# Kernel optimization log

Measured on AMD Instinct MI355X. Metric: run time of the kernel, lower is better.

Reference implementation:

```python
import jax, jax.numpy as jnp
import numpy as np

T, B, M = 2048, 256, 32


def setup_inputs() -> dict:
    key = jax.random.key(0)
    k1, k2, k3, k4 = jax.random.split(key, 4)
    emissions = jax.random.normal(k1, (T, B, M), jnp.float32)
    tags = jax.random.randint(k2, (T, B), 0, M)
    # weight divides transition scores -> keep strictly positive
    weight = jax.random.uniform(k3, (T, B), jnp.float32, 0.5, 1.5)
    mask = jnp.ones((T, B), jnp.int32)  # first timestep must be all-on
    transitions = jax.random.normal(k4, (M, M), jnp.float32) * 0.1
    start_transitions = jnp.zeros((M,), jnp.float32)
    end_transitions = jnp.zeros((M,), jnp.float32)
    return {
        "emissions": emissions,
        "tags": tags,
        "weight": weight,
        "mask": mask,
        "transitions": transitions,
        "start_transitions": start_transitions,
        "end_transitions": end_transitions,
    }


def reference(emissions, tags, weight, mask, transitions, start_transitions, end_transitions):
    # emissions: [T,B,M]; tags/weight/mask: [T,B]; reduction='sum' (torch default)
    Tn, Bn, Mn = emissions.shape
    maskb = mask.astype(bool)
    tags = jnp.where(maskb, tags, 1)
    maskf = mask.astype(emissions.dtype)

    # ---- gold-path score (_compute_score) ----
    score = start_transitions[tags[0]]
    score = score + (transitions[tags[:-1], tags[1:]] * maskf[1:] / weight[:-1]).sum(0)
    em_sc = jnp.take_along_axis(emissions, tags[:, :, None], axis=-1)[..., 0] * maskf
    score = score + em_sc.sum(0)
    seq_ends = mask.astype(jnp.int32).sum(0) - 1  # [B]
    last_tags = tags[seq_ends, jnp.arange(Bn)]
    score = score + end_transitions[last_tags]

    # ---- log-partition (_compute_normalizer) via logsumexp-semiring scan ----
    neg_inf = jnp.asarray(-jnp.inf, emissions.dtype)
    log_eye = jnp.where(jnp.eye(Mn, dtype=bool), jnp.zeros((), emissions.dtype), neg_inf)

    alpha0 = start_transitions + emissions[0]  # [B,M]

    def step(alpha, xs):
        em_t, w_t, m_t = xs  # [B,M], [B], [B]
        sc = transitions[None, :, :] / w_t[:, None, None] + em_t[:, None, :]  # [B,M,M]
        sc = jnp.where(m_t[:, None, None], sc, log_eye)  # masked step = identity in log-semiring
        alpha = jax.nn.logsumexp(alpha[:, :, None] + sc, axis=1)
        return alpha, None

    alpha, _ = jax.lax.scan(step, alpha0, (emissions[1:], weight[:-1], maskb[1:]))
    log_Z = jax.nn.logsumexp(alpha + end_transitions, axis=1)  # [B]

    nllh = log_Z - score
    return nllh.sum()
```

## Files before the change

kernel.cpp:

```cpp
#include <hip/hip_runtime.h>
#include <hip/hip_bf16.h>
#include <stdint.h>


#define T_DIM 2048
#define B_DIM 256
#define M_DIM 32
#define CHUNKS 32
#define CLEN 64
#define KSC 184.6649652337873f
#define SBIAS2 12599160.66f

typedef __attribute__((ext_vector_type(8))) short short8;
typedef __attribute__((ext_vector_type(16))) float f32x16;

__device__ __forceinline__ int pack_bf16(float lo, float hi) {
  union { float f; uint32_t u; } a, b;
  a.f = lo; b.f = hi;
  return (int)__builtin_amdgcn_perm(b.u, a.u, 0x07060302u);
}

__device__ __forceinline__ int pack_lo16(int lo, int hi) {
  return (int)__builtin_amdgcn_perm((uint32_t)hi, (uint32_t)lo, 0x05040100u);
}

__device__ __forceinline__ float bcast_lane(float v, int idx) {
  return __int_as_float(__builtin_amdgcn_readlane(__float_as_int(v), idx));
}

__global__ __launch_bounds__(256, 2) void chunk_kernel(
    const float* __restrict__ em, const int* __restrict__ tags,
    const float* __restrict__ wt, const int* __restrict__ mask,
    const float* __restrict__ trans, const float* __restrict__ endt,
    uint32_t* __restrict__ mats, float* __restrict__ offs,
    float* __restrict__ out)
{
  int tid = threadIdx.x;
  int lane = tid & 63;
  int h = lane >> 5;
  int r = lane & 31;
  int wid = blockIdx.x * 4 + (tid >> 6);
  int u0 = 4 * wid;
  int bb = u0 & (B_DIM - 1);
  int c = u0 >> 8;
  int t0 = 1 + c * CLEN;
  int t1 = t0 + CLEN; if (t1 > T_DIM) t1 = T_DIM;

  float tpre[16];
#pragma unroll
  for (int j = 0; j < 8; ++j) {
    int row = ((j < 4) ? j : j + 4) + 4 * h;
    tpre[j]     = trans[row * 32 + r] * KSC;
    tpre[8 + j] = trans[(row + 16) * 32 + r] * KSC;
  }

  int tw = t0 - 1 + lane; if (tw > T_DIM - 1) tw = T_DIM - 1;
  int tmk = t0 + lane; if (tmk > T_DIM - 1) tmk = T_DIM - 1;
  float rwv[4];
  uint64_t mk[4];
  uint64_t valid = (t1 - t0 >= 64) ? ~0ull : ((1ull << (t1 - t0)) - 1ull);
#pragma unroll
  for (int ch = 0; ch < 4; ++ch) {
    rwv[ch] = __builtin_amdgcn_rcpf(wt[tw * B_DIM + bb + ch]);
    mk[ch] = __ballot(mask[tmk * B_DIM + bb + ch] != 0) & valid;
  }

  f32x16 X[4];
#pragma unroll
  for (int p = 0; p < 16; ++p) {
    float v = (((p & 3) + 8 * (p >> 2) + 4 * h) == r) ? 1.f : 0.f;
    X[0][p] = v; X[1][p] = v; X[2][p] = v; X[3][p] = v;
  }
  f32x16 z;
#pragma unroll
  for (int u = 0; u < 16; ++u) z[u] = 0.f;

  float off2[4] = {0.f, 0.f, 0.f, 0.f};

  auto step4 = [&](const float* e4, int s) {
    float rw0 = bcast_lane(rwv[0], s), rw1 = bcast_lane(rwv[1], s);
    float rw2 = bcast_lane(rwv[2], s), rw3 = bcast_lane(rwv[3], s);
    float rw[4] = {rw0, rw1, rw2, rw3};
    union { int i[4]; short8 s8; } af1[4], af2[4], b1[4], b2[4];
#pragma unroll
    for (int ch = 0; ch < 4; ++ch) {
      float e = fmaf(e4[ch], KSC, SBIAS2);
      float qf[16];
#pragma unroll
      for (int j = 0; j < 16; ++j)
        qf[j] = fmaf(tpre[j], rw[ch], e);
#pragma unroll
      for (int u = 0; u < 4; ++u) {
        af1[ch].i[u] = pack_lo16(__float_as_int(qf[2 * u]),     __float_as_int(qf[2 * u + 1]));
        af2[ch].i[u] = pack_lo16(__float_as_int(qf[8 + 2 * u]), __float_as_int(qf[8 + 2 * u + 1]));
      }
    }
#pragma unroll
    for (int ch = 0; ch < 4; ++ch)
#pragma unroll
      for (int u = 0; u < 4; ++u) {
        b1[ch].i[u] = pack_bf16(X[ch][2 * u],     X[ch][2 * u + 1]);
        b2[ch].i[u] = pack_bf16(X[ch][8 + 2 * u], X[ch][8 + 2 * u + 1]);
      }
    f32x16 d[4];
#pragma unroll
    for (int ch = 0; ch < 4; ++ch)
      d[ch] = __builtin_amdgcn_mfma_f32_32x32x16_bf16(af1[ch].s8, b1[ch].s8, z, 0, 0, 0);
#pragma unroll
    for (int ch = 0; ch < 4; ++ch)
      X[ch] = __builtin_amdgcn_mfma_f32_32x32x16_bf16(af2[ch].s8, b2[ch].s8, d[ch], 0, 0, 0);
  };

  auto stepOne = [&](f32x16& Xc, float e_em, float rw) {
    float e = fmaf(e_em, KSC, SBIAS2);
    float qf[16];
#pragma unroll
    for (int j = 0; j < 16; ++j)
      qf[j] = fmaf(tpre[j], rw, e);
    union { int i[4]; short8 s8; } af1, af2, b1_, b2_;
#pragma unroll
    for (int u = 0; u < 4; ++u) {
      af1.i[u] = pack_lo16(__float_as_int(qf[2 * u]),     __float_as_int(qf[2 * u + 1]));
      af2.i[u] = pack_lo16(__float_as_int(qf[8 + 2 * u]), __float_as_int(qf[8 + 2 * u + 1]));
      b1_.i[u] = pack_bf16(Xc[2 * u],     Xc[2 * u + 1]);
      b2_.i[u] = pack_bf16(Xc[8 + 2 * u], Xc[8 + 2 * u + 1]);
    }
    f32x16 d = __builtin_amdgcn_mfma_f32_32x32x16_bf16(af1.s8, b1_.s8, z, 0, 0, 0);
    Xc = __builtin_amdgcn_mfma_f32_32x32x16_bf16(af2.s8, b2_.s8, d, 0, 0, 0);
  };

  auto rescale = [&](f32x16& Xc, float& o2) {
    float mx = Xc[0];
#pragma unroll
    for (int u = 1; u < 16; ++u) mx = fmaxf(mx, Xc[u]);
#pragma unroll
    for (int off = 1; off < 64; off <<= 1) mx = fmaxf(mx, __shfl_xor(mx, off));
    float sc = __builtin_amdgcn_rcpf(mx);
    o2 += __builtin_amdgcn_logf(mx);
#pragma unroll
    for (int u = 0; u < 16; ++u) Xc[u] *= sc;
  };

  bool fast = (t1 - t0 == 64) && (mk[0] == ~0ull) && (mk[1] == ~0ull)
            && (mk[2] == ~0ull) && (mk[3] == ~0ull);

  if (fast) {
    float e[4][4], n[4][4];
#pragma unroll
    for (int ch = 0; ch < 4; ++ch)
#pragma unroll
      for (int u = 0; u < 4; ++u)
        e[ch][u] = em[((size_t)((t0 + 2 * u + h) * B_DIM + bb + ch)) * 32 + r];
    for (int g = 0; g < 8; ++g) {
      int tg = t0 + 8 * (g + 1);
#pragma unroll
      for (int ch = 0; ch < 4; ++ch)
#pragma unroll
        for (int u = 0; u < 4; ++u) {
          int tt = tg + 2 * u + h; if (tt > T_DIM - 1) tt = T_DIM - 1;
          n[ch][u] = em[((size_t)(tt * B_DIM + bb + ch)) * 32 + r];
        }
#pragma unroll
      for (int u = 0; u < 4; ++u) {
        int sA = 8 * g + 2 * u, sB = sA + 1;
        float eA[4], eB[4];
#pragma unroll
        for (int ch = 0; ch < 4; ++ch) {
          float sw = __shfl_xor(e[ch][u], 32);
          eA[ch] = h ? sw : e[ch][u];
          eB[ch] = h ? e[ch][u] : sw;
        }
        step4(eA, sA);
        step4(eB, sB);
      }
#pragma unroll
      for (int ch = 0; ch < 4; ++ch) rescale(X[ch], off2[ch]);
#pragma unroll
      for (int ch = 0; ch < 4; ++ch)
#pragma unroll
        for (int u = 0; u < 4; ++u) e[ch][u] = n[ch][u];
    }
  } else {
    float emv[4], emp[4];
#pragma unroll
    for (int ch = 0; ch < 4; ++ch)
      emv[ch] = em[((size_t)((t0 + h) * B_DIM + bb + ch)) * 32 + r];
    int tpf = t0 + 2 + h; if (tpf > T_DIM - 1) tpf = T_DIM - 1;
#pragma unroll
    for (int ch = 0; ch < 4; ++ch)
      emp[ch] = em[((size_t)(tpf * B_DIM + bb + ch)) * 32 + r];

    for (int it = 0; it < CLEN / 2; ++it) {
      int tn = t0 + 2 * it + 4 + h; if (tn > T_DIM - 1) tn = T_DIM - 1;
      float emn[4];
#pragma unroll
      for (int ch = 0; ch < 4; ++ch)
        emn[ch] = em[((size_t)(tn * B_DIM + bb + ch)) * 32 + r];

      int sA = 2 * it, sB = sA + 1;
#pragma unroll
      for (int ch = 0; ch < 4; ++ch) {
        float sw = __shfl_xor(emv[ch], 32);
        if ((mk[ch] >> sA) & 1)
          stepOne(X[ch], h ? sw : emv[ch], bcast_lane(rwv[ch], sA));
        if ((t0 + sB < t1) && ((mk[ch] >> sB) & 1))
          stepOne(X[ch], h ? emv[ch] : sw, bcast_lane(rwv[ch], sB));
      }

      if ((it & 3) == 3) {
#pragma unroll
        for (int ch = 0; ch < 4; ++ch) rescale(X[ch], off2[ch]);
      }
#pragma unroll
      for (int ch = 0; ch < 4; ++ch) { emv[ch] = emp[ch]; emp[ch] = emn[ch]; }
    }
  }

#pragma unroll
  for (int ch = 0; ch < 4; ++ch) {
    uint32_t* mp = mats + (size_t)(u0 + ch) * 512;
#pragma unroll
    for (int u = 0; u < 8; ++u) {
      int pairIdx = (u & 1) + (u >> 1) * 4 + 2 * h;
      mp[pairIdx * 32 + r] = (uint32_t)pack_bf16(X[ch][2 * u], X[ch][2 * u + 1]);
    }
  }
  if (lane == 0) {
#pragma unroll
    for (int ch = 0; ch < 4; ++ch) offs[u0 + ch] = off2[ch];
  }

  int t = t0 + lane;
  float ssc = 0.f;
  if (t < t1) {
#pragma unroll
    for (int ch = 0; ch < 4; ++ch) {
      int b = bb + ch;
      int mkc  = mask[t * B_DIM + b];
      int mkn  = (t + 1 < T_DIM) ? mask[(t + 1) * B_DIM + b] : 0;
      int tg   = mkc ? tags[t * B_DIM + b] : 1;
      int mkp  = mask[(t - 1) * B_DIM + b];
      int tgp  = mkp ? tags[(t - 1) * B_DIM + b] : 1;
      if (mkc)
        ssc += em[(size_t)(t * B_DIM + b) * 32 + tg]
             + trans[tgp * 32 + tg] * __builtin_amdgcn_rcpf(wt[(t - 1) * B_DIM + b]);
      if (mkc && !mkn) ssc += endt[tg];
    }
  }
#pragma unroll
  for (int off = 32; off; off >>= 1) ssc += __shfl_xor(ssc, off);
  if (lane == 0) atomicAdd(out, -ssc);
}

__global__ __launch_bounds__(64) void combine_kernel(
    const float* __restrict__ em, const int* __restrict__ tags,
    const int* __restrict__ mask, const float* __restrict__ startt,
    const float* __restrict__ endt, const uint32_t* __restrict__ mats,
    const float* __restrict__ offs, float* __restrict__ out)
{
  const float INV_LN2 = 1.44269504088896340736f;
  const float LN2 = 0.69314718055994530942f;
  int lane = threadIdx.x;
  int j = lane & 31;
  int h = lane >> 5;
  int b = blockIdx.x;
  int jp = j >> 1, jh = j & 1;

  float a0 = (startt[j] + em[(size_t)b * 32 + j]) * INV_LN2;
  float c0 = a0;
#pragma unroll
  for (int off = 1; off < 32; off <<= 1) c0 = fmaxf(c0, __shfl_xor(c0, off));
  float av = __builtin_amdgcn_exp2f(a0 - c0);
  float acc = c0;

  const uint4* xr0 = (const uint4*)(mats + (size_t)b * 512 + jp * 32 + 16 * h);
  uint4 nv0 = xr0[0], nv1 = xr0[1];
  float noff = offs[b];

  for (int c = 0; c < CHUNKS; ++c) {
    uint4 v0 = nv0, v1 = nv1;
    float offc = noff;
    int cn = (c + 1 < CHUNKS) ? c + 1 : c;
    const uint4* xrn = (const uint4*)(mats + (size_t)(cn * B_DIM + b) * 512 + jp * 32 + 16 * h);
    nv0 = xrn[0]; nv1 = xrn[1];
    noff = offs[cn * B_DIM + b];

    float x[8];
    uint32_t u0[4] = {v0.x, v0.y, v0.z, v0.w};
    uint32_t u1[4] = {v1.x, v1.y, v1.z, v1.w};
#pragma unroll
    for (int e = 0; e < 4; ++e) {
      uint32_t bits0 = jh ? (u0[e] & 0xFFFF0000u) : (u0[e] << 16);
      uint32_t bits1 = jh ? (u1[e] & 0xFFFF0000u) : (u1[e] << 16);
      union { uint32_t uu; float f; } cv0, cv1;
      cv0.uu = bits0; cv1.uu = bits1;
      x[e] = cv0.f; x[4 + e] = cv1.f;
    }
    float s0 = 0.f, s1 = 0.f;
#pragma unroll
    for (int i = 0; i < 4; ++i) {
      s0 = fmaf(x[i],     __shfl(av, 16 * h + i),     s0);
      s1 = fmaf(x[4 + i], __shfl(av, 16 * h + 4 + i), s1);
    }
    float an = s0 + s1;
    an += __shfl_xor(an, 32);
    float mx = an;
#pragma unroll
    for (int off = 1; off < 32; off <<= 1) mx = fmaxf(mx, __shfl_xor(mx, off));
    av = an * __builtin_amdgcn_rcpf(mx);
    acc += __builtin_amdgcn_logf(mx) + offc;
  }

  float sv = av * __builtin_amdgcn_exp2f(endt[j] * INV_LN2);
#pragma unroll
  for (int off = 1; off < 32; off <<= 1) sv += __shfl_xor(sv, off);
  if (lane == 0) {
    float logZ = (acc + __builtin_amdgcn_logf(sv)) * LN2;
    int mk0 = mask[b];
    int tg0 = mk0 ? tags[b] : 1;
    float s0 = startt[tg0] + (mk0 ? em[(size_t)b * 32 + tg0] : 0.f);
    int mk1 = mask[B_DIM + b];
    if (mk0 && !mk1) s0 += endt[tg0];
    atomicAdd(out, logZ - s0);
  }
}

extern "C" void kernel_launch(void* const* d_in, const int* in_sizes, int n_in,
                              void* d_out, int out_size, void* d_ws, size_t ws_size,
                              hipStream_t stream) {
  const float* em   = (const float*)d_in[0];
  const int*   tags = (const int*)d_in[1];
  const float* wt   = (const float*)d_in[2];
  const int*   mask = (const int*)d_in[3];
  const float* tr   = (const float*)d_in[4];
  const float* stt  = (const float*)d_in[5];
  const float* ent  = (const float*)d_in[6];
  float* out = (float*)d_out;

  float* offs = (float*)d_ws;
  uint32_t* mats = (uint32_t*)(offs + CHUNKS * B_DIM);

  hipMemsetAsync(out, 0, sizeof(float) * out_size, stream);
  chunk_kernel<<<(CHUNKS * B_DIM) / 16, 256, 0, stream>>>(em, tags, wt, mask, tr, ent, mats, offs, out);
  combine_kernel<<<B_DIM, 64, 0, stream>>>(em, tags, mask, stt, ent, mats, offs, out);
}
```

Measured before the change: 181.6 us.

## Fuse combine stage into chunk kernel via grid-wide atomic counter barrier

Removes the separate combine kernel launch by having the first B_DIM blocks spin-wait on a global completion counter after all chunk blocks finish, then run the cross-chunk combine in the same kernel. A second counter lets block 0 publish the final accumulated sum to the output. This saves one kernel launch and its inter-kernel gap. The cost is a software grid barrier that relies on all 512 blocks being co-resident (2 per CU at 256 threads), which risks deadlock if occupancy drops, and spin-waiting blocks hold CU slots meanwhile.

Result: slower. 320.8 us (+76.6%).

```diff
diff --git a/kernel.cpp b/kernel.cpp
--- a/kernel.cpp
+++ b/kernel.cpp
@@ -8,6 +8,7 @@
 #define M_DIM 32
 #define CHUNKS 32
 #define CLEN 64
+#define NBLOCKS ((CHUNKS * B_DIM) / 16)
 #define KSC 184.6649652337873f
 #define SBIAS2 12599160.66f
 
@@ -28,13 +29,20 @@
   return __int_as_float(__builtin_amdgcn_readlane(__float_as_int(v), idx));
 }
 
+__device__ __forceinline__ uint32_t ld_cnt(uint32_t* p) {
+  return __hip_atomic_load(p, __ATOMIC_RELAXED, __HIP_MEMORY_SCOPE_AGENT);
+}
+
 __global__ __launch_bounds__(256, 2) void chunk_kernel(
     const float* __restrict__ em, const int* __restrict__ tags,
     const float* __restrict__ wt, const int* __restrict__ mask,
-    const float* __restrict__ trans, const float* __restrict__ endt,
-    uint32_t* __restrict__ mats, float* __restrict__ offs,
+    const float* __restrict__ trans, const float* __restrict__ startt,
+    const float* __restrict__ endt,
+    uint32_t* __restrict__ ctrl,
+    float* __restrict__ offs, uint32_t* __restrict__ mats,
     float* __restrict__ out)
 {
+  float* accum = (float*)(ctrl + 2);
   int tid = threadIdx.x;
   int lane = tid & 63;
   int h = lane >> 5;
@@ -249,79 +257,92 @@
   }
 #pragma unroll
   for (int off = 32; off; off >>= 1) ssc += __shfl_xor(ssc, off);
-  if (lane == 0) atomicAdd(out, -ssc);
-}
-
-__global__ __launch_bounds__(64) void combine_kernel(
-    const float* __restrict__ em, const int* __restrict__ tags,
-    const int* __restrict__ mask, const float* __restrict__ startt,
-    const float* __restrict__ endt, const uint32_t* __restrict__ mats,
-    const float* __restrict__ offs, float* __restrict__ out)
-{
-  const float INV_LN2 = 1.44269504088896340736f;
-  const float LN2 = 0.69314718055994530942f;
-  int lane = threadIdx.x;
-  int j = lane & 31;
-  int h = lane >> 5;
-  int b = blockIdx.x;
-  int jp = j >> 1, jh = j & 1;
-
-  float a0 = (startt[j] + em[(size_t)b * 32 + j]) * INV_LN2;
-  float c0 = a0;
-#pragma unroll
-  for (int off = 1; off < 32; off <<= 1) c0 = fmaxf(c0, __shfl_xor(c0, off));
-  float av = __builtin_amdgcn_exp2f(a0 - c0);
-  float acc = c0;
-
-  const uint4* xr0 = (const uint4*)(mats + (size_t)b * 512 + jp * 32 + 16 * h);
-  uint4 nv0 = xr0[0], nv1 = xr0[1];
-  float noff = offs[b];
-
-  for (int c = 0; c < CHUNKS; ++c) {
-    uint4 v0 = nv0, v1 = nv1;
-    float offc = noff;
-    int cn = (c + 1 < CHUNKS) ? c + 1 : c;
-    const uint4* xrn = (const uint4*)(mats + (size_t)(cn * B_DIM + b) * 512 + jp * 32 + 16 * h);
-    nv0 = xrn[0]; nv1 = xrn[1];
-    noff = offs[cn * B_DIM + b];
-
-    float x[8];
-    uint32_t u0[4] = {v0.x, v0.y, v0.z, v0.w};
-    uint32_t u1[4] = {v1.x, v1.y, v1.z, v1.w};
-#pragma unroll
-    for (int e = 0; e < 4; ++e) {
-      uint32_t bits0 = jh ? (u0[e] & 0xFFFF0000u) : (u0[e] << 16);
-      uint32_t bits1 = jh ? (u1[e] & 0xFFFF0000u) : (u1[e] << 16);
-      union { uint32_t uu; float f; } cv0, cv1;
-      cv0.uu = bits0; cv1.uu = bits1;
-      x[e] = cv0.f; x[4 + e] = cv1.f;
-    }
-    float s0 = 0.f, s1 = 0.f;
-#pragma unroll
-    for (int i = 0; i < 4; ++i) {
-      s0 = fmaf(x[i],     __shfl(av, 16 * h + i),     s0);
-      s1 = fmaf(x[4 + i], __shfl(av, 16 * h + 4 + i), s1);
-    }
-    float an = s0 + s1;
-    an += __shfl_xor(an, 32);
-    float mx = an;
-#pragma unroll
-    for (int off = 1; off < 32; off <<= 1) mx = fmaxf(mx, __shfl_xor(mx, off));
-    av = an * __builtin_amdgcn_rcpf(mx);
-    acc += __builtin_amdgcn_logf(mx) + offc;
-  }
-
-  float sv = av * __builtin_amdgcn_exp2f(endt[j] * INV_LN2);
-#pragma unroll
-  for (int off = 1; off < 32; off <<= 1) sv += __shfl_xor(sv, off);
-  if (lane == 0) {
-    float logZ = (acc + __builtin_amdgcn_logf(sv)) * LN2;
-    int mk0 = mask[b];
-    int tg0 = mk0 ? tags[b] : 1;
-    float s0 = startt[tg0] + (mk0 ? em[(size_t)b * 32 + tg0] : 0.f);
-    int mk1 = mask[B_DIM + b];
-    if (mk0 && !mk1) s0 += endt[tg0];
-    atomicAdd(out, logZ - s0);
+  if (lane == 0) atomicAdd(accum, -ssc);
+
+  __syncthreads();
+  if (tid == 0) {
+    __builtin_amdgcn_fence(__ATOMIC_RELEASE, "agent");
+    atomicAdd(&ctrl[0], 1u);
+  }
+
+  if (blockIdx.x >= B_DIM || tid >= 64) return;
+  {
+    while (ld_cnt(&ctrl[0]) < (uint32_t)NBLOCKS) __builtin_amdgcn_s_sleep(8);
+    __builtin_amdgcn_fence(__ATOMIC_ACQUIRE, "agent");
+
+    const float INV_LN2 = 1.44269504088896340736f;
+    const float LN2 = 0.69314718055994530942f;
+    int b = blockIdx.x;
+    int j = lane & 31;
+    int hh = lane >> 5;
+    int jp = j >> 1, jh = j & 1;
+
+    float a0 = (startt[j] + em[(size_t)b * 32 + j]) * INV_LN2;
+    float c0 = a0;
+#pragma unroll
+    for (int off = 1; off < 32; off <<= 1) c0 = fmaxf(c0, __shfl_xor(c0, off));
+    float av = __builtin_amdgcn_exp2f(a0 - c0);
+    float acc = c0;
+
+    const uint4* xr0 = (const uint4*)(mats + (size_t)b * 512 + jp * 32 + 16 * hh);
+    uint4 nv0 = xr0[0], nv1 = xr0[1];
+    float noff = offs[b];
+
+    for (int cc = 0; cc < CHUNKS; ++cc) {
+      uint4 v0 = nv0, v1 = nv1;
+      float offc = noff;
+      int cn = (cc + 1 < CHUNKS) ? cc + 1 : cc;
+      const uint4* xrn = (const uint4*)(mats + (size_t)(cn * B_DIM + b) * 512 + jp * 32 + 16 * hh);
+      nv0 = xrn[0]; nv1 = xrn[1];
+      noff = offs[cn * B_DIM + b];
+
+      float x[8];
+      uint32_t w0[4] = {v0.x, v0.y, v0.z, v0.w};
+      uint32_t w1[4] = {v1.x, v1.y, v1.z, v1.w};
+#pragma unroll
+      for (int e = 0; e < 4; ++e) {
+        uint32_t bits0 = jh ? (w0[e] & 0xFFFF0000u) : (w0[e] << 16);
+        uint32_t bits1 = jh ? (w1[e] & 0xFFFF0000u) : (w1[e] << 16);
+        union { uint32_t uu; float f; } cv0, cv1;
+        cv0.uu = bits0; cv1.uu = bits1;
+        x[e] = cv0.f; x[4 + e] = cv1.f;
+      }
+      float s0 = 0.f, s1 = 0.f;
+#pragma unroll
+      for (int i = 0; i < 4; ++i) {
+        s0 = fmaf(x[i],     __shfl(av, 16 * hh + i),     s0);
+        s1 = fmaf(x[4 + i], __shfl(av, 16 * hh + 4 + i), s1);
+      }
+      float an = s0 + s1;
+      an += __shfl_xor(an, 32);
+      float mx = an;
+#pragma unroll
+      for (int off = 1; off < 32; off <<= 1) mx = fmaxf(mx, __shfl_xor(mx, off));
+      av = an * __builtin_amdgcn_rcpf(mx);
+      acc += __builtin_amdgcn_logf(mx) + offc;
+    }
+
+    float sv = av * __builtin_amdgcn_exp2f(endt[j] * INV_LN2);
+#pragma unroll
+    for (int off = 1; off < 32; off <<= 1) sv += __shfl_xor(sv, off);
+    if (lane == 0) {
+      float logZ = (acc + __builtin_amdgcn_logf(sv)) * LN2;
+      int mk0 = mask[b];
+      int tg0 = mk0 ? tags[b] : 1;
+      float s0 = startt[tg0] + (mk0 ? em[(size_t)b * 32 + tg0] : 0.f);
+      int mk1 = mask[B_DIM + b];
+      if (mk0 && !mk1) s0 += endt[tg0];
+      atomicAdd(accum, logZ - s0);
+      __builtin_amdgcn_fence(__ATOMIC_RELEASE, "agent");
+      atomicAdd(&ctrl[1], 1u);
+    }
+  }
+
+  if (blockIdx.x == 0 && tid == 0) {
+    while (ld_cnt(&ctrl[1]) < (uint32_t)B_DIM) __builtin_amdgcn_s_sleep(8);
+    __builtin_amdgcn_fence(__ATOMIC_ACQUIRE, "agent");
+    out[0] = __hip_atomic_load((float*)(ctrl + 2), __ATOMIC_RELAXED,
+                               __HIP_MEMORY_SCOPE_AGENT);
   }
 }
 
@@ -337,10 +358,11 @@
   const float* ent  = (const float*)d_in[6];
   float* out = (float*)d_out;
 
-  float* offs = (float*)d_ws;
+  uint32_t* ctrl = (uint32_t*)d_ws;
+  float* offs = (float*)d_ws + 4;
   uint32_t* mats = (uint32_t*)(offs + CHUNKS * B_DIM);
 
-  hipMemsetAsync(out, 0, sizeof(float) * out_size, stream);
-  chunk_kernel<<<(CHUNKS * B_DIM) / 16, 256, 0, stream>>>(em, tags, wt, mask, tr, ent, mats, offs, out);
-  combine_kernel<<<B_DIM, 64, 0, stream>>>(em, tags, mask, stt, ent, mats, offs, out);
-}
+  (void)hipMemsetAsync(ctrl, 0, 16, stream);
+  chunk_kernel<<<NBLOCKS, 256, 0, stream>>>(em, tags, wt, mask, tr, stt, ent,
+                                            ctrl, offs, mats, out);
+}
```
